# Optimization experiments

Measured on AMD Instinct MI355X. Metric: run time of the kernel, lower is better.

Reference implementation:

```python
import jax, jax.numpy as jnp
import numpy as np

D_MODEL = 1024
N_HEADS = 16
NUM_KV_HEADS = 4
D_K = D_MODEL // N_HEADS
ROPE_BASE = 10000.0


def apply_rotary_emb(x, base=ROPE_BASE):
    # x: [B, H, T, D], half-split rotation over positions 0..T-1
    B, H, T, D = x.shape
    inv_freq = 1.0 / (base ** (jnp.arange(0, D, 2, dtype=jnp.float32) / D))  # [D/2]
    ang = jnp.arange(T, dtype=jnp.float32)[:, None] * inv_freq[None, :]      # [T, D/2]
    cos = jnp.cos(ang)[None, None].astype(x.dtype)
    sin = jnp.sin(ang)[None, None].astype(x.dtype)
    x1, x2 = x[..., : D // 2], x[..., D // 2 :]
    return jnp.concatenate([x1 * cos - x2 * sin, x2 * cos + x1 * sin], axis=-1)


def setup_inputs() -> dict:
    key = jax.random.key(0)
    ks = jax.random.split(key, 6)
    B, Tq, Tkv = 4, 2048, 2048
    query = jax.random.normal(ks[0], (B, Tq, D_MODEL), dtype=jnp.float32)
    key_value = jax.random.normal(ks[1], (B, Tkv, D_MODEL), dtype=jnp.float32)
    query_mask = jnp.ones((B, Tq), dtype=jnp.bool_)
    kv_mask = jnp.ones((B, Tkv), dtype=jnp.bool_)
    s = 0.02
    w_q = jax.random.normal(ks[2], (D_MODEL, D_MODEL), dtype=jnp.float32) * s
    w_k = jax.random.normal(ks[3], (NUM_KV_HEADS * D_K, D_MODEL), dtype=jnp.float32) * s
    w_v = jax.random.normal(ks[4], (NUM_KV_HEADS * D_K, D_MODEL), dtype=jnp.float32) * s
    w_out = jax.random.normal(ks[5], (D_MODEL, D_MODEL), dtype=jnp.float32) * s
    return {"query": query, "key_value": key_value, "query_mask": query_mask,
            "kv_mask": kv_mask, "w_q": w_q, "w_k": w_k, "w_v": w_v, "w_out": w_out}


def reference(query, key_value, query_mask, kv_mask, w_q, w_k, w_v, w_out):
    B, Tq, _ = query.shape
    Tkv = key_value.shape[1]
    group = N_HEADS // NUM_KV_HEADS
    # projections (torch Linear: x @ W.T)
    Q = (query @ w_q.T).reshape(B, Tq, N_HEADS, D_K).transpose(0, 2, 1, 3)        # [B,H,Tq,D]
    K = (key_value @ w_k.T).reshape(B, Tkv, NUM_KV_HEADS, D_K).transpose(0, 2, 1, 3)
    V = (key_value @ w_v.T).reshape(B, Tkv, NUM_KV_HEADS, D_K).transpose(0, 2, 1, 3)
    # RoPE on Q and K
    Q = apply_rotary_emb(Q)
    K = apply_rotary_emb(K)
    # GQA: repeat kv heads
    K = jnp.repeat(K, group, axis=1)  # [B,H,Tkv,D]
    V = jnp.repeat(V, group, axis=1)
    # mask: [B,1,Tq,Tkv]
    attn_mask = (kv_mask[:, None, None, :] & query_mask[:, None, :, None])
    scale = 1.0 / jnp.sqrt(jnp.asarray(D_K, dtype=Q.dtype))
    scores = jnp.einsum("bhqd,bhkd->bhqk", Q, K) * scale
    scores = jnp.where(attn_mask, scores, jnp.asarray(-jnp.inf, dtype=scores.dtype))
    attn = jax.nn.softmax(scores, axis=-1)
    out = jnp.einsum("bhqk,bhkd->bhqd", attn, V)
    out = out.transpose(0, 2, 1, 3).reshape(B, Tq, D_MODEL)
    out = out @ w_out.T
    return out
```

## Files before the change

kernel.cpp:

```cpp
#include <hip/hip_runtime.h>
#include <hip/hip_bf16.h>
#include <hip/hip_fp16.h>

#define B_    4
#define TQ    2048
#define TKV   2048
#define DM    1024
#define NH    16
#define NKV   4
#define DK    64

typedef _Float16 f16x8 __attribute__((ext_vector_type(8)));
typedef _Float16 f16x4 __attribute__((ext_vector_type(4)));
typedef float    f32x4 __attribute__((ext_vector_type(4)));
typedef float    f32x16 __attribute__((ext_vector_type(16)));

__device__ __forceinline__ void store1(float* p, float v) { *p = v; }
__device__ __forceinline__ void store1(__half* p, float v) {
  union { __half h; unsigned short u; } c; c.h = __float2half(v);
  *(unsigned short*)p = c.u;
}

__device__ __forceinline__ f16x4 load4h(const float* p) {
  float4 v = *(const float4*)p;
  f16x4 r;
  r[0] = (_Float16)v.x; r[1] = (_Float16)v.y;
  r[2] = (_Float16)v.z; r[3] = (_Float16)v.w;
  return r;
}
__device__ __forceinline__ f16x4 load4h(const __half* p) {
  return *(const f16x4*)p;
}

__device__ __forceinline__ unsigned pack2h(float a, float b) {
  auto pk = __builtin_amdgcn_cvt_pkrtz(a, b);
  unsigned u;
  __builtin_memcpy(&u, &pk, 4);
  return u;
}

__global__ void zero_out_kernel(float* out, int n) {
  int i = blockIdx.x * blockDim.x + threadIdx.x;
  if (i < n) out[i] = 0.0f;
}

#define GAP 40
template <typename AT, typename CT>
__global__ __launch_bounds__(256) void gemm_bt_mfma(
    const AT* __restrict__ A,
    const float* __restrict__ W0, const float* __restrict__ W1,
    CT* __restrict__ C0, CT* __restrict__ C1, int M, int N, int K) {
  __shared__ _Float16 As[128 * GAP];
  __shared__ _Float16 Ws[128 * GAP];
  const float* __restrict__ W = (blockIdx.z == 0) ? W0 : W1;
  CT* __restrict__ C = (blockIdx.z == 0) ? C0 : C1;

  const int t = threadIdx.x;
  const int w = t >> 6, l = t & 63;
  const int lm = l & 15, quad = l >> 4;
  const int wm = (w >> 1) * 64, wn = (w & 1) * 64;
  const int m0 = blockIdx.y * 128, n0 = blockIdx.x * 128;

  const int srow = t >> 3;
  const int scol = (t & 7) * 4;

  f32x4 acc[4][4] = {};

  for (int k0 = 0; k0 < K; k0 += 32) {
    f16x4 av[4], wv[4];
#pragma unroll
    for (int p = 0; p < 4; ++p) {
      int r = srow + p * 32;
      av[p] = load4h(&A[(size_t)(m0 + r) * K + k0 + scol]);
      wv[p] = load4h(&W[(size_t)(n0 + r) * K + k0 + scol]);
    }
    __syncthreads();
#pragma unroll
    for (int p = 0; p < 4; ++p) {
      int r = srow + p * 32;
      *(f16x4*)&As[r * GAP + scol] = av[p];
      *(f16x4*)&Ws[r * GAP + scol] = wv[p];
    }
    __syncthreads();

    f16x8 af[4], bf[4];
#pragma unroll
    for (int i = 0; i < 4; ++i)
      af[i] = *(const f16x8*)&As[(wm + i * 16 + lm) * GAP + quad * 8];
#pragma unroll
    for (int j = 0; j < 4; ++j)
      bf[j] = *(const f16x8*)&Ws[(wn + j * 16 + lm) * GAP + quad * 8];
#pragma unroll
    for (int i = 0; i < 4; ++i)
#pragma unroll
      for (int j = 0; j < 4; ++j)
        acc[i][j] =
            __builtin_amdgcn_mfma_f32_16x16x32_f16(af[i], bf[j], acc[i][j], 0, 0, 0);
  }

#pragma unroll
  for (int i = 0; i < 4; ++i)
#pragma unroll
    for (int r = 0; r < 4; ++r) {
      size_t row = (size_t)(m0 + wm + i * 16 + quad * 4 + r) * N;
#pragma unroll
      for (int j = 0; j < 4; ++j)
        store1(&C[row + n0 + wn + j * 16 + lm], acc[i][j][r]);
    }
}

__global__ void rope_kernel(__half* __restrict__ X, int T, int H, int total_pairs) {
  int idx = blockIdx.x * blockDim.x + threadIdx.x;
  if (idx >= total_pairs) return;
  int i   = idx & 31;
  int h   = (idx >> 5) % H;
  int row = idx / (32 * H);
  int tpos = row % T;
  __half* p = X + ((size_t)row * H + h) * DK;
  float inv = exp2f((float)i * -0.41524101186091403f);
  float ang = (float)tpos * inv;
  float c, s;
  sincosf(ang, &s, &c);
  float x1 = __half2float(p[i]), x2 = __half2float(p[i + 32]);
  p[i]      = __float2half(x1 * c - x2 * s);
  p[i + 32] = __float2half(x2 * c + x1 * s);
}

#define AP 72
#define C2 0.18033688011112042f
__global__ __launch_bounds__(256, 2) void attn_mfma(const __half* Q,
                                                    const __half* __restrict__ K,
                                                    const __half* __restrict__ V,
                                                    __half* O) {
  __shared__ _Float16 Ks[64 * AP];
  __shared__ _Float16 Vt[64 * AP];
  const int t = threadIdx.x;
  const int w = t >> 6, l = t & 63;
  const int lq = l & 31, hi = l >> 5;
  const int qt = blockIdx.x, h = blockIdx.y, b = blockIdx.z;
  const int kvh = h >> 2;

  const __half* qbase =
      Q + (((size_t)b * TQ + qt * 128 + w * 32 + lq) * NH + h) * DK;
  f16x8 aq[4];
#pragma unroll
  for (int kc = 0; kc < 4; ++kc)
    aq[kc] = *(const f16x8*)(qbase + kc * 16 + hi * 8);

  const f16x8 vones = {1.f16, 1.f16, 1.f16, 1.f16, 1.f16, 1.f16, 1.f16, 1.f16};

  const int skey = t >> 3, sdseg = t & 7;
  const int vkey = t & 63, vdb0 = (t >> 6) * 8;
  const __half* kp0 =
      K + (((size_t)b * TKV + skey) * NKV + kvh) * DK + sdseg * 8;
  const __half* kp1 = kp0 + (size_t)32 * NKV * DK;
  const __half* vp0 =
      V + (((size_t)b * TKV + vkey) * NKV + kvh) * DK + vdb0;
  const __half* vp1 = vp0 + 32;
  const size_t kstep = (size_t)64 * NKV * DK;

  f16x8 kpre0 = *(const f16x8*)kp0, kpre1 = *(const f16x8*)kp1;
  f16x8 vpre0 = *(const f16x8*)vp0, vpre1 = *(const f16x8*)vp1;

  f32x16 o_acc[2], l_acc;
#pragma unroll
  for (int i = 0; i < 16; ++i) { o_acc[0][i] = 0.f; o_acc[1][i] = 0.f; l_acc[i] = 0.f; }
  float m_run = -1e30f;

  for (int ck = 0; ck < TKV / 64; ++ck) {
    __syncthreads();
    *(f16x8*)&Ks[skey * AP + sdseg * 8] = kpre0;
    *(f16x8*)&Ks[(skey + 32) * AP + sdseg * 8] = kpre1;
#pragma unroll
    for (int j = 0; j < 8; ++j) {
      Vt[(vdb0 + j) * AP + vkey] = vpre0[j];
      Vt[(vdb0 + 32 + j) * AP + vkey] = vpre1[j];
    }
    __syncthreads();
    if (ck + 1 < TKV / 64) {
      size_t off = (size_t)(ck + 1) * kstep;
      kpre0 = *(const f16x8*)(kp0 + off);
      kpre1 = *(const f16x8*)(kp1 + off);
      vpre0 = *(const f16x8*)(vp0 + off);
      vpre1 = *(const f16x8*)(vp1 + off);
    }

    f32x16 st[2];
#pragma unroll
    for (int i = 0; i < 16; ++i) { st[0][i] = 0.f; st[1][i] = 0.f; }
    __builtin_amdgcn_s_setprio(1);
#pragma unroll
    for (int tile = 0; tile < 2; ++tile)
#pragma unroll
      for (int kc = 0; kc < 4; ++kc) {
        f16x8 ak =
            *(const f16x8*)&Ks[(tile * 32 + lq) * AP + kc * 16 + hi * 8];
        st[tile] =
            __builtin_amdgcn_mfma_f32_32x32x16_f16(ak, aq[kc], st[tile], 0, 0, 0);
      }
    __builtin_amdgcn_s_setprio(0);

    float vmax = st[0][0];
#pragma unroll
    for (int i = 1; i < 16; ++i) vmax = fmaxf(vmax, st[0][i]);
#pragma unroll
    for (int i = 0; i < 16; ++i) vmax = fmaxf(vmax, st[1][i]);
    vmax *= C2;
    vmax = fmaxf(vmax, __shfl_xor(vmax, 32));

    if (!__all(vmax - m_run <= 8.0f)) {
      float m_new = fmaxf(m_run, vmax);
      float alpha = exp2f(m_run - m_new);
      m_run = m_new;
#pragma unroll
      for (int reg = 0; reg < 16; ++reg) {
        int row = (reg & 3) + 8 * (reg >> 2) + 4 * hi;
        float ar = __shfl(alpha, row);
        l_acc[reg] *= ar;
        o_acc[0][reg] *= ar;
        o_acc[1][reg] *= ar;
      }
    }

    unsigned q16u[2][8];
#pragma unroll
    for (int tile = 0; tile < 2; ++tile)
#pragma unroll
      for (int rr = 0; rr < 8; ++rr) {
        float p0 = exp2f(st[tile][2 * rr] * C2 - m_run);
        float p1 = exp2f(st[tile][2 * rr + 1] * C2 - m_run);
        q16u[tile][rr] = pack2h(p0, p1);
      }

    __builtin_amdgcn_s_setprio(1);
#pragma unroll
    for (int kb = 0; kb < 4; ++kb) {
      const int tl = kb >> 1, base = (kb & 1) * 4;
      union { unsigned u[4]; f16x8 v; } ap;
#pragma unroll
      for (int c = 0; c < 2; ++c) {
        unsigned R0 = q16u[tl][base + c];
        unsigned R1 = q16u[tl][base + 2 + c];
        unsigned Z = hi ? R0 : R1;
        unsigned Xp = __shfl_xor(Z, 32);
        ap.u[c]     = hi ? Xp : R0;
        ap.u[c + 2] = hi ? R1 : Xp;
      }
      l_acc = __builtin_amdgcn_mfma_f32_32x32x16_f16(ap.v, vones, l_acc, 0, 0, 0);
#pragma unroll
      for (int nt = 0; nt < 2; ++nt) {
        f16x8 bv = *(const f16x8*)&Vt[(nt * 32 + lq) * AP + kb * 16 + hi * 8];
        o_acc[nt] =
            __builtin_amdgcn_mfma_f32_32x32x16_f16(ap.v, bv, o_acc[nt], 0, 0, 0);
      }
    }
    __builtin_amdgcn_s_setprio(0);
  }

#pragma unroll
  for (int reg = 0; reg < 16; ++reg) {
    int row = (reg & 3) + 8 * (reg >> 2) + 4 * hi;
    float inv = 1.0f / l_acc[reg];
    size_t orow =
        (((size_t)b * TQ + qt * 128 + w * 32 + row) * NH + h) * DK;
    O[orow + lq]      = __float2half(o_acc[0][reg] * inv);
    O[orow + 32 + lq] = __float2half(o_acc[1][reg] * inv);
  }
}

extern "C" void kernel_launch(void* const* d_in, const int* in_sizes, int n_in,
                              void* d_out, int out_size, void* d_ws, size_t ws_size,
                              hipStream_t stream) {
  int iq, ikv, iwq, iwk, iwv, iwo;
  bool ok = true;
  if (n_in >= 8 && in_sizes[0] == 8388608 && in_sizes[1] == 8388608) {
    iq = 0; ikv = 1; iwq = 4; iwk = 5; iwv = 6; iwo = 7;
  } else if (n_in >= 8 && in_sizes[0] == 8388608 && in_sizes[1] == 8192) {
    ikv = 0; iq = 2; iwk = 4; iwo = 5; iwq = 6; iwv = 7;
  } else if (n_in == 6 && in_sizes[2] == 1048576) {
    iq = 0; ikv = 1; iwq = 2; iwk = 3; iwv = 4; iwo = 5;
  } else if (n_in == 6 && in_sizes[2] == 262144) {
    ikv = 0; iq = 1; iwk = 2; iwo = 3; iwq = 4; iwv = 5;
  } else {
    ok = false; iq = ikv = iwq = iwk = iwv = iwo = 0;
  }

  const size_t nQ  = (size_t)B_ * TQ * DM;
  const size_t nKV = (size_t)B_ * TKV * NKV * DK;
  const size_t need = (nQ + 2 * nKV) * sizeof(__half);
  if (!ok || ws_size < need) {
    zero_out_kernel<<<(out_size + 255) / 256, 256, 0, stream>>>((float*)d_out,
                                                                out_size);
    return;
  }

  const float* query     = (const float*)d_in[iq];
  const float* key_value = (const float*)d_in[ikv];
  const float* w_q   = (const float*)d_in[iwq];
  const float* w_k   = (const float*)d_in[iwk];
  const float* w_v   = (const float*)d_in[iwv];
  const float* w_out = (const float*)d_in[iwo];
  float* out = (float*)d_out;

  __half* Qh = (__half*)d_ws;
  __half* Kh = Qh + nQ;
  __half* Vh = Kh + nKV;

  dim3 blk(256);
  gemm_bt_mfma<<<dim3(DM / 128, B_ * TQ / 128, 1), blk, 0, stream>>>(
      query, w_q, w_q, Qh, Qh, B_ * TQ, DM, DM);
  gemm_bt_mfma<<<dim3(NKV * DK / 128, B_ * TKV / 128, 2), blk, 0, stream>>>(
      key_value, w_k, w_v, Kh, Vh, B_ * TKV, NKV * DK, DM);
  int pq = B_ * TQ * NH * 32;
  rope_kernel<<<(pq + 255) / 256, blk, 0, stream>>>(Qh, TQ, NH, pq);
  int pk = B_ * TKV * NKV * 32;
  rope_kernel<<<(pk + 255) / 256, blk, 0, stream>>>(Kh, TKV, NKV, pk);
  attn_mfma<<<dim3(TQ / 128, NH, B_), dim3(256), 0, stream>>>(Qh, Kh, Vh, Qh);
  gemm_bt_mfma<<<dim3(DM / 128, B_ * TQ / 128, 1), blk, 0, stream>>>(
      Qh, w_out, w_out, out, out, B_ * TQ, DM, DM);
}
```

Before: 399.8 us.

## Double-buffer GEMM shared tiles and fuse Q RoPE into attention kernel

The GEMM now double-buffers its shared-memory tiles and prefetches the next K-slice into registers while the MFMAs run on the current one, leaving one barrier per iteration instead of two. Separately, RoPE for Q is applied in registers right after the attention kernel loads its Q fragment, which removes a standalone rope pass over Q in global memory. The costs are double the LDS footprint per GEMM block, which may lower occupancy, and per-thread sincos/exp2 work inside the attention kernel.

New measurement: 382.7 us. 1.04x faster.

```diff
diff --git a/kernel.cpp b/kernel.cpp
--- a/kernel.cpp
+++ b/kernel.cpp
@@ -50,8 +50,8 @@
     const AT* __restrict__ A,
     const float* __restrict__ W0, const float* __restrict__ W1,
     CT* __restrict__ C0, CT* __restrict__ C1, int M, int N, int K) {
-  __shared__ _Float16 As[128 * GAP];
-  __shared__ _Float16 Ws[128 * GAP];
+  __shared__ _Float16 As[2 * 128 * GAP];
+  __shared__ _Float16 Ws[2 * 128 * GAP];
   const float* __restrict__ W = (blockIdx.z == 0) ? W0 : W1;
   CT* __restrict__ C = (blockIdx.z == 0) ? C0 : C1;
 
@@ -65,37 +65,48 @@
   const int scol = (t & 7) * 4;
 
   f32x4 acc[4][4] = {};
-
+  f16x4 av[4], wv[4];
+#pragma unroll
+  for (int p = 0; p < 4; ++p) {
+    int r = srow + p * 32;
+    av[p] = load4h(&A[(size_t)(m0 + r) * K + scol]);
+    wv[p] = load4h(&W[(size_t)(n0 + r) * K + scol]);
+  }
+
+  int cur = 0;
   for (int k0 = 0; k0 < K; k0 += 32) {
-    f16x4 av[4], wv[4];
+    _Float16* as = &As[cur * 128 * GAP];
+    _Float16* ws = &Ws[cur * 128 * GAP];
 #pragma unroll
     for (int p = 0; p < 4; ++p) {
       int r = srow + p * 32;
-      av[p] = load4h(&A[(size_t)(m0 + r) * K + k0 + scol]);
-      wv[p] = load4h(&W[(size_t)(n0 + r) * K + k0 + scol]);
+      *(f16x4*)&as[r * GAP + scol] = av[p];
+      *(f16x4*)&ws[r * GAP + scol] = wv[p];
     }
     __syncthreads();
-#pragma unroll
-    for (int p = 0; p < 4; ++p) {
-      int r = srow + p * 32;
-      *(f16x4*)&As[r * GAP + scol] = av[p];
-      *(f16x4*)&Ws[r * GAP + scol] = wv[p];
-    }
-    __syncthreads();
+    if (k0 + 32 < K) {
+#pragma unroll
+      for (int p = 0; p < 4; ++p) {
+        int r = srow + p * 32;
+        av[p] = load4h(&A[(size_t)(m0 + r) * K + k0 + 32 + scol]);
+        wv[p] = load4h(&W[(size_t)(n0 + r) * K + k0 + 32 + scol]);
+      }
+    }
 
     f16x8 af[4], bf[4];
 #pragma unroll
     for (int i = 0; i < 4; ++i)
-      af[i] = *(const f16x8*)&As[(wm + i * 16 + lm) * GAP + quad * 8];
+      af[i] = *(const f16x8*)&as[(wm + i * 16 + lm) * GAP + quad * 8];
 #pragma unroll
     for (int j = 0; j < 4; ++j)
-      bf[j] = *(const f16x8*)&Ws[(wn + j * 16 + lm) * GAP + quad * 8];
+      bf[j] = *(const f16x8*)&ws[(wn + j * 16 + lm) * GAP + quad * 8];
 #pragma unroll
     for (int i = 0; i < 4; ++i)
 #pragma unroll
       for (int j = 0; j < 4; ++j)
         acc[i][j] =
             __builtin_amdgcn_mfma_f32_16x16x32_f16(af[i], bf[j], acc[i][j], 0, 0, 0);
+    cur ^= 1;
   }
 
 #pragma unroll
@@ -147,6 +158,23 @@
   for (int kc = 0; kc < 4; ++kc)
     aq[kc] = *(const f16x8*)(qbase + kc * 16 + hi * 8);
 
+  {
+    const float tpos = (float)(qt * 128 + w * 32 + lq);
+#pragma unroll
+    for (int kc = 0; kc < 2; ++kc)
+#pragma unroll
+      for (int j = 0; j < 8; ++j) {
+        int d = kc * 16 + hi * 8 + j;
+        float inv = exp2f((float)d * -0.41524101186091403f);
+        float ang = tpos * inv;
+        float c, s;
+        sincosf(ang, &s, &c);
+        float x1 = (float)aq[kc][j], x2 = (float)aq[kc + 2][j];
+        aq[kc][j]     = (_Float16)(x1 * c - x2 * s);
+        aq[kc + 2][j] = (_Float16)(x2 * c + x1 * s);
+      }
+  }
+
   const f16x8 vones = {1.f16, 1.f16, 1.f16, 1.f16, 1.f16, 1.f16, 1.f16, 1.f16};
 
   const int skey = t >> 3, sdseg = t & 7;
@@ -311,8 +339,6 @@
       query, w_q, w_q, Qh, Qh, B_ * TQ, DM, DM);
   gemm_bt_mfma<<<dim3(NKV * DK / 128, B_ * TKV / 128, 2), blk, 0, stream>>>(
       key_value, w_k, w_v, Kh, Vh, B_ * TKV, NKV * DK, DM);
-  int pq = B_ * TQ * NH * 32;
-  rope_kernel<<<(pq + 255) / 256, blk, 0, stream>>>(Qh, TQ, NH, pq);
   int pk = B_ * TKV * NKV * 32;
   rope_kernel<<<(pk + 255) / 256, blk, 0, stream>>>(Kh, TKV, NKV, pk);
   attn_mfma<<<dim3(TQ / 128, NH, B_), dim3(256), 0, stream>>>(Qh, Kh, Vh, Qh);
```
